# Performance work log

Measured on AMD Instinct MI355X. Metric: run time of the kernel, lower is better.

Reference implementation:

```python
import jax, jax.numpy as jnp
import numpy as np

N_NODES = 100000
N_EDGES = 1600000
D_IN = 128
D_OUT = 128


def setup_inputs() -> dict:
    key = jax.random.key(0)
    k1, k2, k3, k4 = jax.random.split(key, 4)
    x = jax.random.normal(k1, (N_NODES, D_IN), dtype=jnp.float32)
    edge_index = jax.random.randint(k2, (2, N_EDGES), 0, N_NODES, dtype=jnp.int64)
    # PyTorch Linear default init: U(-1/sqrt(fan_in), 1/sqrt(fan_in))
    bound = 1.0 / np.sqrt(D_IN)
    W1 = jax.random.uniform(k3, (D_OUT, D_IN), minval=-bound, maxval=bound, dtype=jnp.float32)
    W2 = jax.random.uniform(k4, (D_OUT, D_IN), minval=-bound, maxval=bound, dtype=jnp.float32)
    return {"x": x, "edge_index": edge_index, "W1": W1, "W2": W2}


def reference(x, edge_index, W1, W2):
    # self transform: [N, D_out]
    self_features = x @ W1.T
    # neighbor transform: [N, D_out]
    neighbor_features = x @ W2.T
    row, col = edge_index[0], edge_index[1]
    # gather by source (col), scatter-add by destination (row)
    aggregated = jax.ops.segment_sum(neighbor_features[col], row, num_segments=x.shape[0])
    return jax.nn.relu(self_features + aggregated)
```

## Files before the change

### kernel.cpp

```cpp
#include <hip/hip_runtime.h>

#define N_NODES 100000
#define DIM 128
#define NBIN 391
#define BINSZ 256
#define NCH 782
#define CHUNK 2048
#define FCAP 24
#define SLOTS (NBIN * FCAP)
#define ENTCAP 4608
#define FSPB 128
#define LSPB 64
#define NGEMM 782

typedef __attribute__((ext_vector_type(8))) short bf16x8;
typedef __attribute__((ext_vector_type(4))) float f32x4;

__device__ __forceinline__ unsigned short f2bf(float f) {
  unsigned u = __builtin_bit_cast(unsigned, f);
  u += 0x7fff + ((u >> 16) & 1);
  return (unsigned short)(u >> 16);
}
__device__ __forceinline__ float bfhi(unsigned u) {
  return __builtin_bit_cast(float, u & 0xffff0000u);
}
__device__ __forceinline__ float bflo(unsigned u) {
  return __builtin_bit_cast(float, u << 16);
}

__global__ __launch_bounds__(256, 4) void fill_kernel(
    const int* __restrict__ rows, const int* __restrict__ cols,
    int* __restrict__ counts, unsigned* __restrict__ binned,
    int* __restrict__ fspillc, int2* __restrict__ fspill, int n_edges,
    const float* __restrict__ W1, const float* __restrict__ W2,
    unsigned short* __restrict__ Wb) {
  const int tid = threadIdx.x;
  if (blockIdx.x >= NCH) {
    const int v = (blockIdx.x - NCH) * 256 + tid;
    const int j = v >> 5, q = v & 31;
    const float* Wrow =
        (j < 128) ? (W1 + (size_t)j * DIM) : (W2 + (size_t)(j - 128) * DIM);
    const float4 val = *(const float4*)(Wrow + 4 * q);
    const unsigned lo = (unsigned)f2bf(val.x) | ((unsigned)f2bf(val.y) << 16);
    const unsigned hi = (unsigned)f2bf(val.z) | ((unsigned)f2bf(val.w) << 16);
    *(uint2*)(Wb + (size_t)j * DIM + 4 * q) = make_uint2(lo, hi);
    return;
  }

  __shared__ unsigned buf[SLOTS];
  __shared__ int lcnt[NBIN];
  __shared__ int fsc;
  const int ch = blockIdx.x;
  for (int i = tid; i < NBIN; i += 256) lcnt[i] = 0;
  if (tid == 0) fsc = 0;
  __syncthreads();

  const int e0 = ch * CHUNK + tid * 8;
  int rv[8], cv[8];
  int nval;
  if (e0 + 8 <= n_edges) {
    *(int4*)&rv[0] = *(const int4*)(rows + e0);
    *(int4*)&rv[4] = *(const int4*)(rows + e0 + 4);
    *(int4*)&cv[0] = *(const int4*)(cols + e0);
    *(int4*)&cv[4] = *(const int4*)(cols + e0 + 4);
    nval = 8;
  } else {
    nval = 0;
    for (int k = 0; k < 8; ++k)
      if (e0 + k < n_edges) {
        rv[nval] = rows[e0 + k];
        cv[nval] = cols[e0 + k];
        ++nval;
      }
  }
  for (int k = 0; k < nval; ++k) {
    const int r = rv[k];
    const int b = r >> 8;
    const unsigned payload = ((unsigned)(r & 255) << 17) | (unsigned)cv[k];
    const int slot = atomicAdd(&lcnt[b], 1);
    if (slot < FCAP) {
      buf[b * FCAP + slot] = payload;
    } else {
      const int sp = atomicAdd(&fsc, 1);
      if (sp < FSPB) fspill[ch * FSPB + sp] = make_int2(r, cv[k]);
    }
  }
  __syncthreads();

  unsigned* dst = binned + (size_t)ch * SLOTS;
  for (int i4 = tid; i4 < SLOTS / 4; i4 += 256)
    *(uint4*)(dst + 4 * i4) = *(const uint4*)&buf[4 * i4];
  for (int b = tid; b < NBIN; b += 256)
    counts[(size_t)ch * NBIN + b] = min(lcnt[b], FCAP);
  if (tid == 0) fspillc[ch] = min(fsc, FSPB);
}

__global__ __launch_bounds__(256, 2) void gemm_kernel(
    const float* __restrict__ x, const unsigned short* __restrict__ Wb,
    unsigned short* __restrict__ selfb, unsigned short* __restrict__ neigh) {
  __shared__ unsigned short xs[128 * 136];
  const int tid = threadIdx.x;
  const int t = blockIdx.x;
  const int lane = tid & 63;
  const int w = tid >> 6;
  const int nb = t * 128;
  const int quad = lane >> 4;
  const int l15 = lane & 15;

  bf16x8 bfrag[4][4];
#pragma unroll
  for (int nt = 0; nt < 4; ++nt) {
    const int j = w * 64 + nt * 16 + l15;
#pragma unroll
    for (int ks = 0; ks < 4; ++ks)
      bfrag[nt][ks] =
          *(const bf16x8*)(Wb + (size_t)j * DIM + ks * 32 + quad * 8);
  }

#pragma unroll
  for (int half = 0; half < 2; ++half) {
    float4 av[8];
#pragma unroll
    for (int it = 0; it < 8; ++it) {
      const int v = tid + (half * 8 + it) * 256;
      const int m = v >> 5, q = v & 31;
      av[it] = (nb + m < N_NODES)
                   ? *(const float4*)(x + (size_t)(nb + m) * DIM + 4 * q)
                   : make_float4(0.f, 0.f, 0.f, 0.f);
    }
#pragma unroll
    for (int it = 0; it < 8; ++it) {
      const int v = tid + (half * 8 + it) * 256;
      const int m = v >> 5, q = v & 31;
      const unsigned lo =
          (unsigned)f2bf(av[it].x) | ((unsigned)f2bf(av[it].y) << 16);
      const unsigned hi =
          (unsigned)f2bf(av[it].z) | ((unsigned)f2bf(av[it].w) << 16);
      *(uint2*)&xs[m * 136 + 4 * q] = make_uint2(lo, hi);
    }
  }
  __syncthreads();

  f32x4 acc[8][4];
#pragma unroll
  for (int mt = 0; mt < 8; ++mt)
#pragma unroll
    for (int nt = 0; nt < 4; ++nt) acc[mt][nt] = (f32x4){0.f, 0.f, 0.f, 0.f};

#pragma unroll
  for (int ks = 0; ks < 4; ++ks) {
#pragma unroll
    for (int mt = 0; mt < 8; ++mt) {
      const bf16x8 afrag =
          *(const bf16x8*)&xs[(mt * 16 + l15) * 136 + ks * 32 + quad * 8];
#pragma unroll
      for (int nt = 0; nt < 4; ++nt)
        acc[mt][nt] = __builtin_amdgcn_mfma_f32_16x16x32_bf16(
            afrag, bfrag[nt][ks], acc[mt][nt], 0, 0, 0);
    }
  }

#pragma unroll
  for (int h = 0; h < 2; ++h) {
    __syncthreads();
    if ((w >> 1) == h) {
#pragma unroll
      for (int mt = 0; mt < 8; ++mt)
#pragma unroll
        for (int nt = 0; nt < 4; ++nt) {
          const int col = (w & 1) * 64 + nt * 16 + l15;
#pragma unroll
          for (int r = 0; r < 4; ++r)
            xs[(mt * 16 + quad * 4 + r) * 136 + col] = f2bf(acc[mt][nt][r]);
        }
    }
    __syncthreads();
    unsigned short* dst = h ? neigh : selfb;
#pragma unroll
    for (int it = 0; it < 8; ++it) {
      const int v = it * 256 + tid;
      const int row = v >> 4, q = v & 15;
      if (nb + row < N_NODES)
        *(uint4*)(dst + (size_t)(nb + row) * DIM + 8 * q) =
            *(const uint4*)&xs[row * 136 + 8 * q];
    }
  }
}

__global__ __launch_bounds__(1024, 8) void sortagg_kernel(
    const int* __restrict__ counts, const unsigned* __restrict__ binned,
    const unsigned short* __restrict__ neigh,
    const unsigned short* __restrict__ selfb,
    const int* __restrict__ fspillc, const int2* __restrict__ fspill,
    float* __restrict__ out) {
  __shared__ int segc[NCH];
  __shared__ int ssa[NCH];
  __shared__ unsigned entbuf[ENTCAP];
  __shared__ int outb[ENTCAP];
  __shared__ int hist[BINSZ], hsa[BINSZ], cur[BINSZ];
  __shared__ unsigned lspill[LSPB];
  __shared__ int lsc, tot, hasf;

  const int tid = threadIdx.x;
  const int bin = blockIdx.x;

  if (tid == 0) {
    lsc = 0;
    hasf = 0;
  }
  if (tid < BINSZ) hist[tid] = 0;
  for (int i = tid; i < NCH; i += 1024) {
    const int c = counts[(size_t)i * NBIN + bin];
    segc[i] = c;
    ssa[i] = c;
    if (fspillc[i]) atomicOr(&hasf, 1);
  }
  __syncthreads();

  for (int off = 1; off < NCH; off <<= 1) {
    int add = 0;
    if (tid < NCH && tid >= off) add = ssa[tid - off];
    __syncthreads();
    if (tid < NCH && tid >= off) ssa[tid] += add;
    __syncthreads();
  }
  if (tid == 0) tot = min(ssa[NCH - 1], ENTCAP);

  const unsigned* bbase = binned + (size_t)bin * FCAP;
  for (int u = tid; u < NCH * (FCAP / 4); u += 1024) {
    const int ch = u / 6;
    const int q = u - ch * 6;
    uint4 v4 = *(const uint4*)(bbase + (size_t)ch * SLOTS + 4 * q);
    const int cnt = segc[ch];
    const int base = ssa[ch] - cnt;
    const unsigned vals[4] = {v4.x, v4.y, v4.z, v4.w};
#pragma unroll
    for (int j = 0; j < 4; ++j) {
      const int slot = 4 * q + j;
      if (slot < cnt) {
        const int pos = base + slot;
        if (pos < ENTCAP) {
          outb[0] = outb[0];
          entbuf[pos] = vals[j];
        } else {
          const int sp = atomicAdd(&lsc, 1);
          if (sp < LSPB) lspill[sp] = vals[j];
        }
      }
    }
  }
  __syncthreads();

  if (hasf) {
    for (int bi = tid; bi < NCH; bi += 1024) {
      const int n = min(fspillc[bi], FSPB);
      for (int i = 0; i < n; ++i) {
        const int2 e = fspill[bi * FSPB + i];
        if ((e.x >> 8) == bin) {
          const unsigned pay = ((unsigned)(e.x & 255) << 17) | (unsigned)e.y;
          const int pos = atomicAdd(&tot, 1);
          if (pos < ENTCAP) {
            entbuf[pos] = pay;
          } else {
            const int sp = atomicAdd(&lsc, 1);
            if (sp < LSPB) lspill[sp] = pay;
          }
        }
      }
    }
    __syncthreads();
  }
  const int total = min(tot, ENTCAP);

  for (int i = tid; i < total; i += 1024)
    atomicAdd(&hist[entbuf[i] >> 17], 1);
  __syncthreads();
  if (tid < BINSZ) hsa[tid] = hist[tid];
  __syncthreads();
  for (int off = 1; off < BINSZ; off <<= 1) {
    int add = 0;
    if (tid < BINSZ && tid >= off) add = hsa[tid - off];
    __syncthreads();
    if (tid < BINSZ && tid >= off) hsa[tid] += add;
    __syncthreads();
  }
  if (tid < BINSZ) cur[tid] = hsa[tid] - hist[tid];
  __syncthreads();

  for (int i = tid; i < total; i += 1024) {
    const unsigned p = entbuf[i];
    const int pos = atomicAdd(&cur[p >> 17], 1);
    outb[pos] = (int)(p & 0x1FFFFu);
  }
  __syncthreads();

  const int l = tid & 63;
  const int wv = tid >> 6;
  const unsigned* ng = (const unsigned*)neigh;
  const unsigned* sfp = (const unsigned*)selfb;
  const int nspill = min(lsc, LSPB);

  for (int k = 0; k < 16; ++k) {
    const int nl = wv * 16 + k;
    const int node = (bin << 8) | nl;
    if (node >= N_NODES) break;
    const int deg = hist[nl];
    const int start = hsa[nl] - hist[nl];
    const unsigned s = sfp[(size_t)node * 64 + l];

    float ax = 0.f, ay = 0.f;
    int d = 0;
    for (; d + 8 <= deg; d += 8) {
      unsigned uv[8];
#pragma unroll
      for (int j = 0; j < 8; ++j) uv[j] = ng[(size_t)outb[start + d + j] * 64 + l];
#pragma unroll
      for (int j = 0; j < 8; ++j) {
        ax += bflo(uv[j]);
        ay += bfhi(uv[j]);
      }
    }
    const int rem = deg - d;
    if (rem) {
      unsigned uv[8];
      const int cdup = outb[start + d];
#pragma unroll
      for (int j = 0; j < 8; ++j) {
        const int ci = (j < rem) ? outb[start + d + j] : cdup;
        uv[j] = ng[(size_t)ci * 64 + l];
      }
#pragma unroll
      for (int j = 0; j < 8; ++j) {
        if (j < rem) {
          ax += bflo(uv[j]);
          ay += bfhi(uv[j]);
        }
      }
    }

    for (int i = 0; i < nspill; ++i) {
      const unsigned p = lspill[i];
      if ((int)(p >> 17) == nl) {
        const unsigned u = ng[(size_t)(p & 0x1FFFFu) * 64 + l];
        ax += bflo(u);
        ay += bfhi(u);
      }
    }

    float2 o;
    o.x = fmaxf(bflo(s) + ax, 0.f);
    o.y = fmaxf(bfhi(s) + ay, 0.f);
    *(float2*)(out + (size_t)node * DIM + 2 * l) = o;
  }
}

extern "C" void kernel_launch(void* const* d_in, const int* in_sizes, int n_in,
                              void* d_out, int out_size, void* d_ws,
                              size_t ws_size, hipStream_t stream) {
  const float* x = (const float*)d_in[0];
  const int* edge_index = (const int*)d_in[1];
  const float* W1 = (const float*)d_in[2];
  const float* W2 = (const float*)d_in[3];
  float* out = (float*)d_out;

  const int n_edges = in_sizes[1] / 2;
  const int* rows = edge_index;
  const int* cols = edge_index + n_edges;

  char* p = (char*)d_ws;
  unsigned short* selfb = (unsigned short*)p;
  p += (size_t)N_NODES * DIM * 2;
  unsigned short* neigh = (unsigned short*)p;
  p += (size_t)N_NODES * DIM * 2;
  unsigned* binned = (unsigned*)p;
  p += (size_t)NCH * SLOTS * 4;
  int* counts = (int*)p;
  p += (size_t)NCH * NBIN * 4;
  p += (size_t)NBIN * ENTCAP * 4;
  p += (size_t)N_NODES * 4;
  p += (size_t)N_NODES * 4;
  int* fspillc = (int*)p;
  p += 4096;
  int2* fspill = (int2*)p;
  p += (size_t)NCH * FSPB * sizeof(int2);
  p += 4096;
  p += (size_t)NBIN * 256 * sizeof(int2);
  unsigned short* Wb = (unsigned short*)p;

  fill_kernel<<<NCH + 32, 256, 0, stream>>>(rows, cols, counts, binned,
                                            fspillc, fspill, n_edges, W1, W2,
                                            Wb);
  gemm_kernel<<<NGEMM, 256, 0, stream>>>(x, Wb, selfb, neigh);
  sortagg_kernel<<<NBIN, 1024, 0, stream>>>(counts, binned, neigh, selfb,
                                            fspillc, fspill, out);
}
```

Measured before the change: 217.6 us.

## Merge edge-binning and GEMM into one kernel with interleaved block roles

```diff
diff --git a/kernel.cpp b/kernel.cpp
--- a/kernel.cpp
+++ b/kernel.cpp
@@ -28,161 +28,172 @@
   return __builtin_bit_cast(float, u << 16);
 }
 
-__global__ __launch_bounds__(256, 4) void fill_kernel(
+union FgSh {
+  struct {
+    unsigned buf[SLOTS];
+    int lcnt[NBIN];
+    int fsc;
+  } f;
+  unsigned short xs[128 * 136];
+};
+
+__global__ __launch_bounds__(256, 2) void fillgemm_kernel(
     const int* __restrict__ rows, const int* __restrict__ cols,
     int* __restrict__ counts, unsigned* __restrict__ binned,
     int* __restrict__ fspillc, int2* __restrict__ fspill, int n_edges,
-    const float* __restrict__ W1, const float* __restrict__ W2,
-    unsigned short* __restrict__ Wb) {
+    const float* __restrict__ x, const float* __restrict__ W1,
+    const float* __restrict__ W2, unsigned short* __restrict__ selfb,
+    unsigned short* __restrict__ neigh) {
+  __shared__ FgSh sh;
   const int tid = threadIdx.x;
-  if (blockIdx.x >= NCH) {
-    const int v = (blockIdx.x - NCH) * 256 + tid;
-    const int j = v >> 5, q = v & 31;
-    const float* Wrow =
-        (j < 128) ? (W1 + (size_t)j * DIM) : (W2 + (size_t)(j - 128) * DIM);
-    const float4 val = *(const float4*)(Wrow + 4 * q);
-    const unsigned lo = (unsigned)f2bf(val.x) | ((unsigned)f2bf(val.y) << 16);
-    const unsigned hi = (unsigned)f2bf(val.z) | ((unsigned)f2bf(val.w) << 16);
-    *(uint2*)(Wb + (size_t)j * DIM + 4 * q) = make_uint2(lo, hi);
-    return;
-  }
-
-  __shared__ unsigned buf[SLOTS];
-  __shared__ int lcnt[NBIN];
-  __shared__ int fsc;
-  const int ch = blockIdx.x;
-  for (int i = tid; i < NBIN; i += 256) lcnt[i] = 0;
-  if (tid == 0) fsc = 0;
-  __syncthreads();
-
-  const int e0 = ch * CHUNK + tid * 8;
-  int rv[8], cv[8];
-  int nval;
-  if (e0 + 8 <= n_edges) {
-    *(int4*)&rv[0] = *(const int4*)(rows + e0);
-    *(int4*)&rv[4] = *(const int4*)(rows + e0 + 4);
-    *(int4*)&cv[0] = *(const int4*)(cols + e0);
-    *(int4*)&cv[4] = *(const int4*)(cols + e0 + 4);
-    nval = 8;
+  const int pair = blockIdx.x >> 1;
+
+  if ((blockIdx.x & 1) == 0) {
+    const int ch = pair;
+    for (int i = tid; i < NBIN; i += 256) sh.f.lcnt[i] = 0;
+    if (tid == 0) sh.f.fsc = 0;
+    __syncthreads();
+
+    const int e0 = ch * CHUNK + tid * 8;
+    int rv[8], cv[8];
+    int nval;
+    if (e0 + 8 <= n_edges) {
+      *(int4*)&rv[0] = *(const int4*)(rows + e0);
+      *(int4*)&rv[4] = *(const int4*)(rows + e0 + 4);
+      *(int4*)&cv[0] = *(const int4*)(cols + e0);
+      *(int4*)&cv[4] = *(const int4*)(cols + e0 + 4);
+      nval = 8;
+    } else {
+      nval = 0;
+      for (int k = 0; k < 8; ++k)
+        if (e0 + k < n_edges) {
+          rv[nval] = rows[e0 + k];
+          cv[nval] = cols[e0 + k];
+          ++nval;
+        }
+    }
+    for (int k = 0; k < nval; ++k) {
+      const int r = rv[k];
+      const int b = r >> 8;
+      const unsigned payload = ((unsigned)(r & 255) << 17) | (unsigned)cv[k];
+      const int slot = atomicAdd(&sh.f.lcnt[b], 1);
+      if (slot < FCAP) {
+        sh.f.buf[b * FCAP + slot] = payload;
+      } else {
+        const int sp = atomicAdd(&sh.f.fsc, 1);
+        if (sp < FSPB) fspill[ch * FSPB + sp] = make_int2(r, cv[k]);
+      }
+    }
+    __syncthreads();
+
+    unsigned* dst = binned + (size_t)ch * SLOTS;
+    for (int i4 = tid; i4 < SLOTS / 4; i4 += 256)
+      *(uint4*)(dst + 4 * i4) = *(const uint4*)&sh.f.buf[4 * i4];
+    for (int b = tid; b < NBIN; b += 256)
+      counts[(size_t)ch * NBIN + b] = min(sh.f.lcnt[b], FCAP);
+    if (tid == 0) fspillc[ch] = min(sh.f.fsc, FSPB);
   } else {
-    nval = 0;
-    for (int k = 0; k < 8; ++k)
-      if (e0 + k < n_edges) {
-        rv[nval] = rows[e0 + k];
-        cv[nval] = cols[e0 + k];
-        ++nval;
-      }
-  }
-  for (int k = 0; k < nval; ++k) {
-    const int r = rv[k];
-    const int b = r >> 8;
-    const unsigned payload = ((unsigned)(r & 255) << 17) | (unsigned)cv[k];
-    const int slot = atomicAdd(&lcnt[b], 1);
-    if (slot < FCAP) {
-      buf[b * FCAP + slot] = payload;
-    } else {
-      const int sp = atomicAdd(&fsc, 1);
-      if (sp < FSPB) fspill[ch * FSPB + sp] = make_int2(r, cv[k]);
-    }
-  }
-  __syncthreads();
-
-  unsigned* dst = binned + (size_t)ch * SLOTS;
-  for (int i4 = tid; i4 < SLOTS / 4; i4 += 256)
-    *(uint4*)(dst + 4 * i4) = *(const uint4*)&buf[4 * i4];
-  for (int b = tid; b < NBIN; b += 256)
-    counts[(size_t)ch * NBIN + b] = min(lcnt[b], FCAP);
-  if (tid == 0) fspillc[ch] = min(fsc, FSPB);
-}
-
-__global__ __launch_bounds__(256, 2) void gemm_kernel(
-    const float* __restrict__ x, const unsigned short* __restrict__ Wb,
-    unsigned short* __restrict__ selfb, unsigned short* __restrict__ neigh) {
-  __shared__ unsigned short xs[128 * 136];
-  const int tid = threadIdx.x;
-  const int t = blockIdx.x;
-  const int lane = tid & 63;
-  const int w = tid >> 6;
-  const int nb = t * 128;
-  const int quad = lane >> 4;
-  const int l15 = lane & 15;
-
-  bf16x8 bfrag[4][4];
-#pragma unroll
-  for (int nt = 0; nt < 4; ++nt) {
-    const int j = w * 64 + nt * 16 + l15;
-#pragma unroll
-    for (int ks = 0; ks < 4; ++ks)
-      bfrag[nt][ks] =
-          *(const bf16x8*)(Wb + (size_t)j * DIM + ks * 32 + quad * 8);
-  }
-
-#pragma unroll
-  for (int half = 0; half < 2; ++half) {
-    float4 av[8];
-#pragma unroll
-    for (int it = 0; it < 8; ++it) {
-      const int v = tid + (half * 8 + it) * 256;
-      const int m = v >> 5, q = v & 31;
-      av[it] = (nb + m < N_NODES)
-                   ? *(const float4*)(x + (size_t)(nb + m) * DIM + 4 * q)
-                   : make_float4(0.f, 0.f, 0.f, 0.f);
-    }
-#pragma unroll
-    for (int it = 0; it < 8; ++it) {
-      const int v = tid + (half * 8 + it) * 256;
-      const int m = v >> 5, q = v & 31;
-      const unsigned lo =
-          (unsigned)f2bf(av[it].x) | ((unsigned)f2bf(av[it].y) << 16);
-      const unsigned hi =
-          (unsigned)f2bf(av[it].z) | ((unsigned)f2bf(av[it].w) << 16);
-      *(uint2*)&xs[m * 136 + 4 * q] = make_uint2(lo, hi);
-    }
-  }
-  __syncthreads();
-
-  f32x4 acc[8][4];
-#pragma unroll
-  for (int mt = 0; mt < 8; ++mt)
-#pragma unroll
-    for (int nt = 0; nt < 4; ++nt) acc[mt][nt] = (f32x4){0.f, 0.f, 0.f, 0.f};
-
-#pragma unroll
-  for (int ks = 0; ks < 4; ++ks) {
-#pragma unroll
-    for (int mt = 0; mt < 8; ++mt) {
-      const bf16x8 afrag =
-          *(const bf16x8*)&xs[(mt * 16 + l15) * 136 + ks * 32 + quad * 8];
-#pragma unroll
-      for (int nt = 0; nt < 4; ++nt)
-        acc[mt][nt] = __builtin_amdgcn_mfma_f32_16x16x32_bf16(
-            afrag, bfrag[nt][ks], acc[mt][nt], 0, 0, 0);
-    }
-  }
-
-#pragma unroll
-  for (int h = 0; h < 2; ++h) {
-    __syncthreads();
-    if ((w >> 1) == h) {
-#pragma unroll
-      for (int mt = 0; mt < 8; ++mt)
-#pragma unroll
-        for (int nt = 0; nt < 4; ++nt) {
-          const int col = (w & 1) * 64 + nt * 16 + l15;
-#pragma unroll
-          for (int r = 0; r < 4; ++r)
-            xs[(mt * 16 + quad * 4 + r) * 136 + col] = f2bf(acc[mt][nt][r]);
-        }
-    }
-    __syncthreads();
-    unsigned short* dst = h ? neigh : selfb;
-#pragma unroll
-    for (int it = 0; it < 8; ++it) {
-      const int v = it * 256 + tid;
-      const int row = v >> 4, q = v & 15;
-      if (nb + row < N_NODES)
-        *(uint4*)(dst + (size_t)(nb + row) * DIM + 8 * q) =
-            *(const uint4*)&xs[row * 136 + 8 * q];
+    const int t = pair;
+    const int lane = tid & 63;
+    const int w = tid >> 6;
+    const int nb = t * 128;
+    const int quad = lane >> 4;
+    const int l15 = lane & 15;
+
+    bf16x8 bfrag[4][4];
+#pragma unroll
+    for (int nt = 0; nt < 4; ++nt) {
+      const int j = w * 64 + nt * 16 + l15;
+      const float* Wrow =
+          (j < 128) ? (W1 + (size_t)j * DIM) : (W2 + (size_t)(j - 128) * DIM);
+#pragma unroll
+      for (int ks = 0; ks < 4; ++ks) {
+        const float4 a = *(const float4*)(Wrow + ks * 32 + quad * 8);
+        const float4 b = *(const float4*)(Wrow + ks * 32 + quad * 8 + 4);
+        union {
+          bf16x8 v;
+          unsigned short u[8];
+        } tmp;
+        tmp.u[0] = f2bf(a.x);
+        tmp.u[1] = f2bf(a.y);
+        tmp.u[2] = f2bf(a.z);
+        tmp.u[3] = f2bf(a.w);
+        tmp.u[4] = f2bf(b.x);
+        tmp.u[5] = f2bf(b.y);
+        tmp.u[6] = f2bf(b.z);
+        tmp.u[7] = f2bf(b.w);
+        bfrag[nt][ks] = tmp.v;
+      }
+    }
+
+#pragma unroll
+    for (int half = 0; half < 2; ++half) {
+      float4 av[8];
+#pragma unroll
+      for (int it = 0; it < 8; ++it) {
+        const int v = tid + (half * 8 + it) * 256;
+        const int m = v >> 5, q = v & 31;
+        av[it] = (nb + m < N_NODES)
+                     ? *(const float4*)(x + (size_t)(nb + m) * DIM + 4 * q)
+                     : make_float4(0.f, 0.f, 0.f, 0.f);
+      }
+#pragma unroll
+      for (int it = 0; it < 8; ++it) {
+        const int v = tid + (half * 8 + it) * 256;
+        const int m = v >> 5, q = v & 31;
+        const unsigned lo =
+            (unsigned)f2bf(av[it].x) | ((unsigned)f2bf(av[it].y) << 16);
+        const unsigned hi =
+            (unsigned)f2bf(av[it].z) | ((unsigned)f2bf(av[it].w) << 16);
+        *(uint2*)&sh.xs[m * 136 + 4 * q] = make_uint2(lo, hi);
+      }
+    }
+    __syncthreads();
+
+    f32x4 acc[8][4];
+#pragma unroll
+    for (int mt = 0; mt < 8; ++mt)
+#pragma unroll
+      for (int nt = 0; nt < 4; ++nt) acc[mt][nt] = (f32x4){0.f, 0.f, 0.f, 0.f};
+
+#pragma unroll
+    for (int ks = 0; ks < 4; ++ks) {
+#pragma unroll
+      for (int mt = 0; mt < 8; ++mt) {
+        const bf16x8 afrag =
+            *(const bf16x8*)&sh.xs[(mt * 16 + l15) * 136 + ks * 32 + quad * 8];
+#pragma unroll
+        for (int nt = 0; nt < 4; ++nt)
+          acc[mt][nt] = __builtin_amdgcn_mfma_f32_16x16x32_bf16(
+              afrag, bfrag[nt][ks], acc[mt][nt], 0, 0, 0);
+      }
+    }
+
+#pragma unroll
+    for (int h = 0; h < 2; ++h) {
+      __syncthreads();
+      if ((w >> 1) == h) {
+#pragma unroll
+        for (int mt = 0; mt < 8; ++mt)
+#pragma unroll
+          for (int nt = 0; nt < 4; ++nt) {
+            const int col = (w & 1) * 64 + nt * 16 + l15;
+#pragma unroll
+            for (int r = 0; r < 4; ++r)
+              sh.xs[(mt * 16 + quad * 4 + r) * 136 + col] =
+                  f2bf(acc[mt][nt][r]);
+          }
+      }
+      __syncthreads();
+      unsigned short* dst = h ? neigh : selfb;
+#pragma unroll
+      for (int it = 0; it < 8; ++it) {
+        const int v = it * 256 + tid;
+        const int row = v >> 4, q = v & 15;
+        if (nb + row < N_NODES)
+          *(uint4*)(dst + (size_t)(nb + row) * DIM + 8 * q) =
+              *(const uint4*)&sh.xs[row * 136 + 8 * q];
+      }
     }
   }
 }
@@ -240,7 +251,6 @@
       if (slot < cnt) {
         const int pos = base + slot;
         if (pos < ENTCAP) {
-          outb[0] = outb[0];
           entbuf[pos] = vals[j];
         } else {
           const int sp = atomicAdd(&lsc, 1);
@@ -313,7 +323,8 @@
     for (; d + 8 <= deg; d += 8) {
       unsigned uv[8];
 #pragma unroll
-      for (int j = 0; j < 8; ++j) uv[j] = ng[(size_t)outb[start + d + j] * 64 + l];
+      for (int j = 0; j < 8; ++j)
+        uv[j] = ng[(size_t)outb[start + d + j] * 64 + l];
 #pragma unroll
       for (int j = 0; j < 8; ++j) {
         ax += bflo(uv[j]);
@@ -383,14 +394,10 @@
   p += 4096;
   int2* fspill = (int2*)p;
   p += (size_t)NCH * FSPB * sizeof(int2);
-  p += 4096;
-  p += (size_t)NBIN * 256 * sizeof(int2);
-  unsigned short* Wb = (unsigned short*)p;
-
-  fill_kernel<<<NCH + 32, 256, 0, stream>>>(rows, cols, counts, binned,
-                                            fspillc, fspill, n_edges, W1, W2,
-                                            Wb);
-  gemm_kernel<<<NGEMM, 256, 0, stream>>>(x, Wb, selfb, neigh);
+
+  fillgemm_kernel<<<2 * NCH, 256, 0, stream>>>(rows, cols, counts, binned,
+                                               fspillc, fspill, n_edges, x,
+                                               W1, W2, selfb, neigh);
   sortagg_kernel<<<NBIN, 1024, 0, stream>>>(counts, binned, neigh, selfb,
                                             fspillc, fspill, out);
 }
```

New measurement: 225.9 us. +3.8%, slower.
